# Kernel optimization log

Hardware: AMD Instinct MI355X
Metric: run time of the kernel (lower is better)

Reference implementation:

```python
import jax, jax.numpy as jnp
import numpy as np

H, DK, DV = 16, 128, 128
BINS = 64
EPS = 1e-6
NORM_EPS = 1e-5


def silu(x):
    return x * jax.nn.sigmoid(x)


def short_conv(x, w):
    # causal depthwise conv over time + silu. x: [B,T,C], w: [C,K]
    C = x.shape[-1]
    K = w.shape[1]
    lhs = jnp.swapaxes(x, 1, 2)              # [B,C,T]
    rhs = w[:, None, :]                      # [C,1,K]
    out = jax.lax.conv_general_dilated(
        lhs, rhs, window_strides=(1,), padding=[(K - 1, 0)],
        dimension_numbers=('NCH', 'OIH', 'NCH'), feature_group_count=C)
    return silu(jnp.swapaxes(out, 1, 2))


def delta_rule(q, k, v, beta, decay):
    # gated delta-rule linear attention recurrence.
    # q,k: [B,T,H,DK], v: [B,T,H,DV], beta: [B,T,H], decay: [B,T,H,DK]
    B = q.shape[0]

    def step(S, inp):
        qt, kt, vt, bt, gt = inp             # [B,H,DK],...,[B,H],[B,H,DK]
        Sd = S * gt[..., None]               # per-key-channel decay
        v_pred = jnp.einsum('bhk,bhkv->bhv', kt, Sd)
        S_new = Sd + jnp.einsum('bhk,bhv->bhkv', kt * bt[..., None], vt - v_pred)
        ot = jnp.einsum('bhk,bhkv->bhv', qt, S_new)
        return S_new, ot

    tm = lambda a: jnp.swapaxes(a, 0, 1)     # time-major
    S0 = jnp.zeros((B, H, DK, DV), q.dtype)
    _, o = jax.lax.scan(step, S0, (tm(q), tm(k), tm(v), tm(beta), tm(decay)))
    return jnp.swapaxes(o, 0, 1)             # [B,T,H,DV]


def _forward(hidden_states, wq, wk, wv, conv_q_w, conv_k_w, conv_v_w, A_log, dt_bias,
             proxy_w, unc_w, head_embed, mlp_w1, mlp_b1, mlp_w2, mlp_b2,
             bb_w, bb_b, bd_w, bd_b, lam_w, lam_b, ab_w, ab_b, ad_w, ad_b,
             g1_w, g2_w, g2_b, onorm_w, wo):
    x = hidden_states
    B, T, _ = x.shape
    q = short_conv(x @ wq, conv_q_w).reshape(B, T, H, DK)
    k = short_conv(x @ wk, conv_k_w).reshape(B, T, H, DK)
    v = short_conv(x @ wv, conv_v_w).reshape(B, T, H, DV)

    # uncertainty (entropy of predicted-token distribution proxy)
    logp = jax.nn.log_softmax(x @ unc_w, axis=-1)
    entropy = -jnp.sum(jnp.exp(logp) * logp, axis=-1)              # [B,T]
    ent_norm = entropy / jnp.log(jnp.asarray(BINS, x.dtype))

    # beta-norm: unit-norm keys inside the kernel
    k_unit = k / (jnp.linalg.norm(k, axis=-1, keepdims=True) + EPS)

    # proxy-value surprise features, per head/token
    v_hat = jnp.einsum('bthk,kv->bthv', k, proxy_w)
    err = v - v_hat
    err_n = jnp.linalg.norm(err, axis=-1)                          # [B,T,H]
    v_n = jnp.linalg.norm(v, axis=-1)
    vh_n = jnp.linalg.norm(v_hat, axis=-1)
    rel_err = err_n / (v_n + EPS)
    cos = jnp.sum(v * v_hat, axis=-1) / (v_n * vh_n + EPS)
    feats = jnp.stack([jnp.broadcast_to(ent_norm[..., None], err_n.shape),
                       rel_err, cos, jnp.log1p(err_n)], axis=-1)    # [B,T,H,4]
    he = jnp.broadcast_to(head_embed[None, None], (B, T, H, head_embed.shape[-1]))
    feats = jnp.concatenate([feats, he], axis=-1)                   # [B,T,H,8]

    hf = silu(silu(feats @ mlp_w1 + mlp_b1) @ mlp_w2 + mlp_b2)      # [B,T,H,32]
    beta_base = hf @ bb_w + bb_b[0]
    beta_delta = hf @ bd_w + bd_b[0]
    beta_fast = jax.nn.sigmoid(beta_base + beta_delta)              # fast memory: bigger step
    beta_slow = jax.nn.sigmoid(beta_base - beta_delta)              # slow memory: smaller step
    lam = jax.nn.sigmoid(hf @ lam_w + lam_b[0])                     # mixing gate
    amp_base = hf @ ab_w + ab_b[0]
    amp_delta = hf @ ad_w + ad_b[0]
    amp_fast = jax.nn.sigmoid(amp_base + amp_delta)
    amp_slow = jax.nn.sigmoid(amp_base - amp_delta)

    # KDA-style per-key-channel log-decay: g = -exp(A_log) * softplus(dt_bias)
    g_chan = -jnp.exp(A_log)[:, None] * jax.nn.softplus(dt_bias).reshape(H, DK)
    decay_fast = jnp.exp(g_chan[None, None] * amp_fast[..., None])  # [B,T,H,DK]
    decay_slow = jnp.exp(g_chan[None, None] * amp_slow[..., None])

    qs = q * (DK ** -0.5)
    o_fast = delta_rule(qs, k_unit, v, beta_fast, decay_fast)
    o_slow = delta_rule(qs, k_unit, v, beta_slow, decay_slow)
    o = lam[..., None] * o_fast + (1.0 - lam[..., None]) * o_slow   # [B,T,H,DV]

    # gated RMSNorm (sigmoid gate) + output projection
    g = ((x @ g1_w) @ g2_w + g2_b).reshape(B, T, H, DV)
    rms = jnp.sqrt(jnp.mean(o * o, axis=-1, keepdims=True) + NORM_EPS)
    o = (o / rms) * onorm_w * jax.nn.sigmoid(g)
    return o.reshape(B, T, H * DV) @ wo


def setup_inputs() -> dict:
    key = jax.random.key(0)
    ks = jax.random.split(key, 40)
    B, T, D = 2, 256, 2048

    def w(k, shape, fan_in):
        return jax.random.normal(k, shape, jnp.float32) * (fan_in ** -0.5)

    return {
        'hidden_states': jax.random.normal(ks[0], (B, T, D), jnp.float32),
        'wq': w(ks[1], (D, H * DK), D),
        'wk': w(ks[2], (D, H * DK), D),
        'wv': w(ks[3], (D, H * DV), D),
        'conv_q_w': w(ks[4], (H * DK, 4), 4),
        'conv_k_w': w(ks[5], (H * DK, 4), 4),
        'conv_v_w': w(ks[6], (H * DV, 4), 4),
        'A_log': jnp.log(jax.random.uniform(ks[7], (H,), jnp.float32, 1.0, 16.0)),
        'dt_bias': jnp.zeros((H * DK,), jnp.float32),
        'proxy_w': w(ks[8], (DK, DV), DK),
        'unc_w': w(ks[9], (D, BINS), D),
        'head_embed': jax.random.normal(ks[10], (H, 4), jnp.float32),
        'mlp_w1': w(ks[11], (8, 32), 8),
        'mlp_b1': jnp.zeros((32,), jnp.float32),
        'mlp_w2': w(ks[12], (32, 32), 32),
        'mlp_b2': jnp.zeros((32,), jnp.float32),
        'bb_w': w(ks[13], (32,), 32), 'bb_b': jnp.zeros((1,), jnp.float32),
        'bd_w': w(ks[14], (32,), 32), 'bd_b': jnp.zeros((1,), jnp.float32),
        'lam_w': w(ks[15], (32,), 32), 'lam_b': jnp.zeros((1,), jnp.float32),
        'ab_w': w(ks[16], (32,), 32), 'ab_b': jnp.zeros((1,), jnp.float32),
        'ad_w': w(ks[17], (32,), 32), 'ad_b': jnp.zeros((1,), jnp.float32),
        'g1_w': w(ks[18], (D, DV), D),
        'g2_w': w(ks[19], (DV, H * DV), DV),
        'g2_b': jnp.zeros((H * DV,), jnp.float32),
        'onorm_w': jnp.ones((DV,), jnp.float32),
        'wo': w(ks[20], (H * DV, D), H * DV),
    }


def reference(hidden_states, wq, wk, wv, conv_q_w, conv_k_w, conv_v_w, A_log, dt_bias,
              proxy_w, unc_w, head_embed, mlp_w1, mlp_b1, mlp_w2, mlp_b2,
              bb_w, bb_b, bd_w, bd_b, lam_w, lam_b, ab_w, ab_b, ad_w, ad_b,
              g1_w, g2_w, g2_b, onorm_w, wo):
    return _forward(hidden_states, wq, wk, wv, conv_q_w, conv_k_w, conv_v_w, A_log,
                    dt_bias, proxy_w, unc_w, head_embed, mlp_w1, mlp_b1, mlp_w2, mlp_b2,
                    bb_w, bb_b, bd_w, bd_b, lam_w, lam_b, ab_w, ab_b, ad_w, ad_b,
                    g1_w, g2_w, g2_b, onorm_w, wo)
```

## Files before the change

### kernel.cpp

```cpp
#include <hip/hip_runtime.h>
#include <hip/hip_bf16.h>
#include <math.h>

#define H_ 16
#define DK_ 128
#define DV_ 128
#define D_ 2048
#define T_ 256
#define B_ 2
#define BT_ 512

typedef __attribute__((ext_vector_type(8))) short short8v;
typedef __attribute__((ext_vector_type(4))) float float4v;
typedef unsigned short ushort_t;

__device__ __forceinline__ float sigmoidf_(float x){ return 1.f/(1.f+expf(-x)); }
__device__ __forceinline__ float siluf_(float x){ return x/(1.f+expf(-x)); }
__device__ __forceinline__ ushort_t f2bf(float f){
    __hip_bfloat16 h = __float2bfloat16(f);
    return *reinterpret_cast<ushort_t*>(&h);
}
__device__ __forceinline__ int swz(int row, int k){
    return row * 32 + ((((k >> 3) ^ (row & 3)) << 3) | (k & 7));
}

template<int CTRL>
__device__ __forceinline__ float ror_add_(float x){
    return x + __int_as_float(__builtin_amdgcn_update_dpp(
        0, __float_as_int(x), CTRL, 0xF, 0xF, true));
}
__device__ __forceinline__ float rsum16_(float x){
    x = ror_add_<0x121>(x);
    x = ror_add_<0x122>(x);
    x = ror_add_<0x124>(x);
    x = ror_add_<0x128>(x);
    return x;
}

__global__ void cvt_gchan(const float* __restrict__ in, ushort_t* __restrict__ out, int n,
                          const float* __restrict__ A_log, const float* __restrict__ dt_bias,
                          float* __restrict__ gchan)
{
    int bid = blockIdx.x;
    if (bid < 1024) {
        int i = (bid * 256 + threadIdx.x) * 4;
        if (i >= n) return;
        float4 v = *(const float4*)&in[i];
        union { ushort_t s[4]; unsigned long long u; } p;
        p.s[0] = f2bf(v.x); p.s[1] = f2bf(v.y); p.s[2] = f2bf(v.z); p.s[3] = f2bf(v.w);
        *(unsigned long long*)&out[i] = p.u;
    } else {
        int i = (bid - 1024) * 256 + threadIdx.x;
        int h = i >> 7;
        float x = dt_bias[i];
        float sp = (x > 20.f) ? x : log1pf(expf(x));
        gchan[i] = -expf(A_log[h]) * sp * 1.44269504088896f;
    }
}

__device__ __forceinline__ void gemm_core(
    const ushort_t* __restrict__ A, int K,
    const float* __restrict__ W, int Nst, int nloc0,
    float* __restrict__ C, int Cst, int m0, int n0out)
{
    __shared__ ushort_t Asub[2048];
    __shared__ ushort_t Bsub[2048];
    const int tid = threadIdx.x;
    const int wid = tid >> 6, lane = tid & 63;
    const int wr = (wid >> 1) * 32, wc = (wid & 1) * 32;
    const int lr = lane & 15, lk = (lane >> 4) * 8;
    const int rowA = tid >> 2, kqA = tid & 3;
    const int nW = tid & 63, kqW = tid >> 6;

    float4v acc[2][2];
    #pragma unroll
    for (int i = 0; i < 2; ++i)
        #pragma unroll
        for (int j = 0; j < 2; ++j) acc[i][j] = (float4v){0.f, 0.f, 0.f, 0.f};

    short8v aRa, aRb;
    float wRa[8], wRb[8];

#define LOADT(AR, WR, KOFF) do {                                                   \
    AR = *(const short8v*)&A[(size_t)(m0 + rowA) * K + (KOFF) + kqA * 8];          \
    _Pragma("unroll")                                                              \
    for (int r = 0; r < 8; ++r)                                                    \
        WR[r] = W[(size_t)((KOFF) + kqW * 8 + r) * Nst + nloc0 + nW];              \
} while (0)
#define STORET(AR, WR) do {                                                        \
    *(short8v*)&Asub[swz(rowA, kqA * 8)] = AR;                                     \
    union { ushort_t s[8]; short8v v; } pk;                                        \
    _Pragma("unroll")                                                              \
    for (int r = 0; r < 8; ++r) pk.s[r] = f2bf(WR[r]);                             \
    *(short8v*)&Bsub[swz(nW, kqW * 8)] = pk.v;                                     \
} while (0)
#define FRAGMMA() do {                                                             \
    short8v af0 = *(const short8v*)&Asub[swz(wr + lr, lk)];                        \
    short8v af1 = *(const short8v*)&Asub[swz(wr + 16 + lr, lk)];                   \
    short8v bf0 = *(const short8v*)&Bsub[swz(wc + lr, lk)];                        \
    short8v bf1 = *(const short8v*)&Bsub[swz(wc + 16 + lr, lk)];                   \
    acc[0][0] = __builtin_amdgcn_mfma_f32_16x16x32_bf16(af0, bf0, acc[0][0],0,0,0);\
    acc[0][1] = __builtin_amdgcn_mfma_f32_16x16x32_bf16(af0, bf1, acc[0][1],0,0,0);\
    acc[1][0] = __builtin_amdgcn_mfma_f32_16x16x32_bf16(af1, bf0, acc[1][0],0,0,0);\
    acc[1][1] = __builtin_amdgcn_mfma_f32_16x16x32_bf16(af1, bf1, acc[1][1],0,0,0);\
} while (0)

    LOADT(aRa, wRa, 0);
    for (int k0 = 0; k0 < K; k0 += 64) {
        STORET(aRa, wRa);
        __syncthreads();
        if (k0 + 32 < K) LOADT(aRb, wRb, k0 + 32);
        FRAGMMA();
        __syncthreads();
        STORET(aRb, wRb);
        __syncthreads();
        if (k0 + 64 < K) LOADT(aRa, wRa, k0 + 64);
        FRAGMMA();
        __syncthreads();
    }
#undef LOADT
#undef STORET
#undef FRAGMMA
    const int lq = (lane >> 4) * 4;
    #pragma unroll
    for (int mi = 0; mi < 2; ++mi)
        #pragma unroll
        for (int ni = 0; ni < 2; ++ni)
            #pragma unroll
            for (int j = 0; j < 4; ++j)
                C[(size_t)(m0 + wr + mi * 16 + lq + j) * Cst + (n0out + wc + ni * 16 + lr)]
                    = acc[mi][ni][j];
}

__device__ __forceinline__ void gemm_core2(
    const ushort_t* __restrict__ A, int K,
    const float* __restrict__ W, int Nst, int nloc0,
    float* __restrict__ C, int Cst, int m0, int n0out)
{
    __shared__ ushort_t Asub[8192];
    __shared__ ushort_t Bsub[2048];
    const int tid = threadIdx.x;
    const int wid = tid >> 6, lane = tid & 63;
    const int wr = wid * 32;
    const int lr = lane & 15, lk = (lane >> 4) * 8;
    const int rowA = tid >> 2;
    const int kqA  = (tid & 3) * 8;
    const int nW = tid & 63, kqW = (tid >> 6) & 3;
    const bool doW = tid < 256;

    float4v acc[2][4];
    #pragma unroll
    for (int i = 0; i < 2; ++i)
        #pragma unroll
        for (int j = 0; j < 4; ++j) acc[i][j] = (float4v){0.f, 0.f, 0.f, 0.f};

    short8v a0a, a1a, a0b, a1b;
    float wRa[8], wRb[8];

#define LOADT2(A0, A1, WR, KOFF) do {                                              \
    A0 = *(const short8v*)&A[(size_t)(m0 + rowA) * K + (KOFF) + kqA];              \
    A1 = *(const short8v*)&A[(size_t)(m0 + rowA + 128) * K + (KOFF) + kqA];        \
    if (doW) {                                                                     \
        _Pragma("unroll")                                                          \
        for (int r = 0; r < 8; ++r)                                                \
            WR[r] = W[(size_t)((KOFF) + kqW * 8 + r) * Nst + nloc0 + nW];          \
    }                                                                              \
} while (0)
#define STORET2(A0, A1, WR) do {                                                   \
    *(short8v*)&Asub[swz(rowA, kqA)] = A0;                                         \
    *(short8v*)&Asub[swz(rowA + 128, kqA)] = A1;                                   \
    if (doW) {                                                                     \
        union { ushort_t s[8]; short8v v; } pk;                                    \
        _Pragma("unroll")                                                          \
        for (int r = 0; r < 8; ++r) pk.s[r] = f2bf(WR[r]);                         \
        *(short8v*)&Bsub[swz(nW, kqW * 8)] = pk.v;                                 \
    }                                                                              \
} while (0)
#define FRAGMMA2() do {                                                            \
    short8v af0 = *(const short8v*)&Asub[swz(wr + lr, lk)];                        \
    short8v af1 = *(const short8v*)&Asub[swz(wr + 16 + lr, lk)];                   \
    short8v bf0 = *(const short8v*)&Bsub[swz(lr, lk)];                             \
    short8v bf1 = *(const short8v*)&Bsub[swz(16 + lr, lk)];                        \
    short8v bf2 = *(const short8v*)&Bsub[swz(32 + lr, lk)];                        \
    short8v bf3 = *(const short8v*)&Bsub[swz(48 + lr, lk)];                        \
    acc[0][0] = __builtin_amdgcn_mfma_f32_16x16x32_bf16(af0, bf0, acc[0][0],0,0,0);\
    acc[0][1] = __builtin_amdgcn_mfma_f32_16x16x32_bf16(af0, bf1, acc[0][1],0,0,0);\
    acc[0][2] = __builtin_amdgcn_mfma_f32_16x16x32_bf16(af0, bf2, acc[0][2],0,0,0);\
    acc[0][3] = __builtin_amdgcn_mfma_f32_16x16x32_bf16(af0, bf3, acc[0][3],0,0,0);\
    acc[1][0] = __builtin_amdgcn_mfma_f32_16x16x32_bf16(af1, bf0, acc[1][0],0,0,0);\
    acc[1][1] = __builtin_amdgcn_mfma_f32_16x16x32_bf16(af1, bf1, acc[1][1],0,0,0);\
    acc[1][2] = __builtin_amdgcn_mfma_f32_16x16x32_bf16(af1, bf2, acc[1][2],0,0,0);\
    acc[1][3] = __builtin_amdgcn_mfma_f32_16x16x32_bf16(af1, bf3, acc[1][3],0,0,0);\
} while (0)

    LOADT2(a0a, a1a, wRa, 0);
    for (int k0 = 0; k0 < K; k0 += 64) {
        STORET2(a0a, a1a, wRa);
        __syncthreads();
        if (k0 + 32 < K) LOADT2(a0b, a1b, wRb, k0 + 32);
        FRAGMMA2();
        __syncthreads();
        STORET2(a0b, a1b, wRb);
        __syncthreads();
        if (k0 + 64 < K) LOADT2(a0a, a1a, wRa, k0 + 64);
        FRAGMMA2();
        __syncthreads();
    }
#undef LOADT2
#undef STORET2
#undef FRAGMMA2
    const int lq = (lane >> 4) * 4;
    #pragma unroll
    for (int mi = 0; mi < 2; ++mi)
        #pragma unroll
        for (int ni = 0; ni < 4; ++ni)
            #pragma unroll
            for (int j = 0; j < 4; ++j)
                C[(size_t)(m0 + wr + mi * 16 + lq + j) * Cst + (n0out + ni * 16 + lr)]
                    = acc[mi][ni][j];
}

__global__ __launch_bounds__(512) void gemm_proj(const ushort_t* __restrict__ A,
    const float* __restrict__ wq, const float* __restrict__ wk, const float* __restrict__ wv,
    const float* __restrict__ unc, const float* __restrict__ g1, float* __restrict__ C)
{
    int n0 = blockIdx.x * 64, m0 = blockIdx.y * 256;
    const float* W; int nloc, Nst;
    if (n0 < 2048)      { W = wq;  nloc = n0;        Nst = 2048; }
    else if (n0 < 4096) { W = wk;  nloc = n0 - 2048; Nst = 2048; }
    else if (n0 < 6144) { W = wv;  nloc = n0 - 4096; Nst = 2048; }
    else if (n0 < 6208) { W = unc; nloc = n0 - 6144; Nst = 64; }
    else                { W = g1;  nloc = n0 - 6208; Nst = 128; }
    gemm_core2(A, 2048, W, Nst, nloc, C, 6336, m0, n0);
}

__global__ __launch_bounds__(256) void gemm_one(const ushort_t* __restrict__ A,
    const float* __restrict__ W, float* __restrict__ C, int N, int K)
{
    gemm_core(A, K, W, N, blockIdx.x * 64, C, N, blockIdx.y * 64, blockIdx.x * 64);
}

__global__ __launch_bounds__(256) void gemm_g2(const float* __restrict__ Cb,
    const float* __restrict__ W, float* __restrict__ C)
{
    __shared__ ushort_t Asub[2048];
    __shared__ ushort_t Bsub[2048];
    const int tid = threadIdx.x;
    const int wid = tid >> 6, lane = tid & 63;
    const int wr = (wid >> 1) * 32, wc = (wid & 1) * 32;
    const int lr = lane & 15, lk = (lane >> 4) * 8;
    const int rowA = tid >> 2, kqA = (tid & 3) * 8;
    const int nW = tid & 63, kqW = tid >> 6;
    const int m0 = blockIdx.y * 64, n0 = blockIdx.x * 64;

    float4v acc[2][2];
    #pragma unroll
    for (int i = 0; i < 2; ++i)
        #pragma unroll
        for (int j = 0; j < 2; ++j) acc[i][j] = (float4v){0.f, 0.f, 0.f, 0.f};

    for (int k0 = 0; k0 < 128; k0 += 32) {
        const float* asrc = &Cb[(size_t)(m0 + rowA) * 6336 + 6208 + k0 + kqA];
        float4 a4a = *(const float4*)asrc;
        float4 a4b = *(const float4*)(asrc + 4);
        float w8[8];
        #pragma unroll
        for (int r = 0; r < 8; ++r)
            w8[r] = W[(size_t)(k0 + kqW * 8 + r) * 2048 + n0 + nW];
        __syncthreads();
        union { ushort_t s[8]; short8v v; } pa, pw;
        pa.s[0]=f2bf(a4a.x); pa.s[1]=f2bf(a4a.y); pa.s[2]=f2bf(a4a.z); pa.s[3]=f2bf(a4a.w);
        pa.s[4]=f2bf(a4b.x); pa.s[5]=f2bf(a4b.y); pa.s[6]=f2bf(a4b.z); pa.s[7]=f2bf(a4b.w);
        *(short8v*)&Asub[swz(rowA, kqA)] = pa.v;
        #pragma unroll
        for (int r = 0; r < 8; ++r) pw.s[r] = f2bf(w8[r]);
        *(short8v*)&Bsub[swz(nW, kqW * 8)] = pw.v;
        __syncthreads();
        short8v af0 = *(const short8v*)&Asub[swz(wr + lr, lk)];
        short8v af1 = *(const short8v*)&Asub[swz(wr + 16 + lr, lk)];
        short8v bf0 = *(const short8v*)&Bsub[swz(wc + lr, lk)];
        short8v bf1 = *(const short8v*)&Bsub[swz(wc + 16 + lr, lk)];
        acc[0][0] = __builtin_amdgcn_mfma_f32_16x16x32_bf16(af0, bf0, acc[0][0],0,0,0);
        acc[0][1] = __builtin_amdgcn_mfma_f32_16x16x32_bf16(af0, bf1, acc[0][1],0,0,0);
        acc[1][0] = __builtin_amdgcn_mfma_f32_16x16x32_bf16(af1, bf0, acc[1][0],0,0,0);
        acc[1][1] = __builtin_amdgcn_mfma_f32_16x16x32_bf16(af1, bf1, acc[1][1],0,0,0);
    }
    const int lq = (lane >> 4) * 4;
    #pragma unroll
    for (int mi = 0; mi < 2; ++mi)
        #pragma unroll
        for (int ni = 0; ni < 2; ++ni)
            #pragma unroll
            for (int j = 0; j < 4; ++j)
                C[(size_t)(m0 + wr + mi * 16 + lq + j) * 2048 + (n0 + wc + ni * 16 + lr)]
                    = acc[mi][ni][j];
}

__global__ void conv_fused(const float* __restrict__ Cb,
    const float* __restrict__ wq, const float* __restrict__ wk, const float* __restrict__ wv,
    float* __restrict__ qc, float* __restrict__ kc, float* __restrict__ vc,
    ushort_t* __restrict__ kcb, float qscale)
{
    int c  = blockIdx.x * 256 + threadIdx.x;
    int bt = blockIdx.y;
    int b  = bt / T_, t = bt % T_;
    int which = c >> 11, cloc = c & 2047;
    const float* w = which == 0 ? wq : which == 1 ? wk : wv;
    float* o = which == 0 ? qc : which == 1 ? kc : vc;
    float scale = which == 0 ? qscale : 1.f;
    float acc = 0.f;
    #pragma unroll
    for (int j = 0; j < 4; ++j) {
        int tt = t - 3 + j;
        if (tt >= 0) acc = fmaf(w[cloc * 4 + j], Cb[((size_t)(b * T_ + tt)) * 6336 + c], acc);
    }
    float r = siluf_(acc) * scale;
    o[(size_t)bt * D_ + cloc] = r;
    if (which == 1) kcb[(size_t)bt * D_ + cloc] = f2bf(r);
}

__global__ __launch_bounds__(128) void featsprec_k(
    const float* __restrict__ kc, const float* __restrict__ vc,
    const float* __restrict__ qc,
    const float* __restrict__ vhatA, const float* __restrict__ Cb,
    const float* __restrict__ he, const float* __restrict__ gchan,
    const float* __restrict__ w1, const float* __restrict__ b1,
    const float* __restrict__ w2, const float* __restrict__ b2,
    const float* __restrict__ bbw, const float* __restrict__ bbb,
    const float* __restrict__ bdw, const float* __restrict__ bdb,
    const float* __restrict__ lamw, const float* __restrict__ lamb,
    const float* __restrict__ abw, const float* __restrict__ abb,
    const float* __restrict__ adw, const float* __restrict__ adb,
    float* __restrict__ lm, float* __restrict__ kuA,
    float* __restrict__ dA, float4* __restrict__ scal4A)
{
    int blk = blockIdx.x;
    int h = blk & 15, bt = blk >> 4;
    int b = bt / T_, t = bt % T_;
    int v = threadIdx.x;
    __shared__ float part[2][5];
    __shared__ float tot5[5];
    __shared__ float feats8[8];
    __shared__ float hf1[32];
    __shared__ float hf[32];
    __shared__ float entSh;
    __shared__ float scal5[5];

    if (v < 64) {
        float x = Cb[(size_t)bt * 6336 + 6144 + v];
        float m = x;
        #pragma unroll
        for (int o = 32; o > 0; o >>= 1) m = fmaxf(m, __shfl_xor(m, o));
        float e = expf(x - m);
        float s = e;
        #pragma unroll
        for (int o = 32; o > 0; o >>= 1) s += __shfl_xor(s, o);
        float lp = (x - m) - logf(s);
        float c = -expf(lp) * lp;
        #pragma unroll
        for (int o = 32; o > 0; o >>= 1) c += __shfl_xor(c, o);
        if (v == 0) entSh = c / logf(64.f);
    }

    size_t base = (size_t)bt * D_ + h * 128;
    float kval = kc[base + v];
    float vval = vc[base + v];
    float vhat = vhatA[(size_t)blk * 128 + v];

    float e = vval - vhat;
    float sums[5] = {kval * kval, vval * vval, vhat * vhat, vval * vhat, e * e};
    #pragma unroll
    for (int i = 0; i < 5; ++i) {
        float s = sums[i];
        #pragma unroll
        for (int o = 32; o > 0; o >>= 1) s += __shfl_xor(s, o);
        if ((threadIdx.x & 63) == 0) part[threadIdx.x >> 6][i] = s;
    }
    __syncthreads();
    if (threadIdx.x < 5) tot5[threadIdx.x] = part[0][threadIdx.x] + part[1][threadIdx.x];
    __syncthreads();
    if (threadIdx.x == 0) {
        float k2 = tot5[0], v2 = tot5[1], vh2 = tot5[2], vvh = tot5[3], e2 = tot5[4];
        float knorm = sqrtf(k2);
        float err_n = sqrtf(e2);
        float v_n = sqrtf(v2);
        float vh_n = sqrtf(vh2);
        feats8[0] = entSh;
        feats8[1] = err_n / (v_n + 1e-6f);
        feats8[2] = vvh / (v_n * vh_n + 1e-6f);
        feats8[3] = log1pf(err_n);
        feats8[4] = he[h * 4 + 0];
        feats8[5] = he[h * 4 + 1];
        feats8[6] = he[h * 4 + 2];
        feats8[7] = he[h * 4 + 3];
        scal5[4] = knorm;
    }
    __syncthreads();
    if (threadIdx.x < 32) {
        float a = b1[threadIdx.x];
        #pragma unroll
        for (int j = 0; j < 8; ++j) a = fmaf(feats8[j], w1[j * 32 + threadIdx.x], a);
        hf1[threadIdx.x] = siluf_(a);
    }
    __syncthreads();
    if (threadIdx.x < 32) {
        float a = b2[threadIdx.x];
        #pragma unroll
        for (int j = 0; j < 32; ++j) a = fmaf(hf1[j], w2[j * 32 + threadIdx.x], a);
        hf[threadIdx.x] = siluf_(a);
    }
    __syncthreads();
    if (threadIdx.x == 0) {
        float bb = bbb[0], bd = bdb[0], lv = lamb[0], ab = abb[0], ad = adb[0];
        #pragma unroll
        for (int j = 0; j < 32; ++j) {
            float hj = hf[j];
            bb = fmaf(hj, bbw[j], bb);
            bd = fmaf(hj, bdw[j], bd);
            lv = fmaf(hj, lamw[j], lv);
            ab = fmaf(hj, abw[j], ab);
            ad = fmaf(hj, adw[j], ad);
        }
        scal5[0] = sigmoidf_(bb + bd);
        scal5[1] = sigmoidf_(bb - bd);
        scal5[2] = sigmoidf_(ab + ad);
        scal5[3] = sigmoidf_(ab - ad);
        lm[((size_t)(b * H_ + h)) * T_ + t] = sigmoidf_(lv);
    }
    __syncthreads();

    const float bfv = scal5[0], bsv = scal5[1];
    const float afv = scal5[2], asv = scal5[3], knv = scal5[4];
    const int k = threadIdx.x;
    const int bh = b * 16 + h;
    float gch = gchan[h * 128 + k];
    float kuv = kval / (knv + 1e-6f);
    kuA[((size_t)bh * 256 + t) * 128 + k] = kuv;
    dA[((size_t)bh * 256 + t) * 128 + k]        = exp2f(gch * afv);
    dA[((size_t)(32 + bh) * 256 + t) * 128 + k] = exp2f(gch * asv);
    float pq = qc[base + k] * kuv;
    #pragma unroll
    for (int o = 32; o > 0; o >>= 1) pq += __shfl_xor(pq, o);
    if ((threadIdx.x & 63) == 0) part[threadIdx.x >> 6][0] = pq;
    __syncthreads();
    if (threadIdx.x == 0) {
        float pt = part[0][0] + part[1][0];
        float4 s0; s0.x = afv; s0.y = bfv; s0.z = pt * bfv; s0.w = 0.f;
        float4 s1; s1.x = asv; s1.y = bsv; s1.z = pt * bsv; s1.w = 0.f;
        scal4A[(size_t)bh * 256 + t] = s0;
        scal4A[(size_t)(32 + bh) * 256 + t] = s1;
    }
}

struct OPS { float4 a0, a1, q0, q1, d0, d1, sc; float2 vv; };

__global__ __launch_bounds__(256) void delta_wave9(
    const float* __restrict__ qc, const float* __restrict__ vc,
    const float* __restrict__ kuA, const float* __restrict__ dA,
    const float4* __restrict__ scal4A,
    float* __restrict__ o_fast, float* __restrict__ o_slow)
{
    const int p  = blockIdx.x;
    const int lb = (p & 7) * 32 + (p >> 3);
    const int bh = lb >> 3, rule = (lb >> 2) & 1, vq = lb & 3;
    const int b = bh >> 4, h = bh & 15;
    const int rbh = rule * 32 + bh;
    const int tid = threadIdx.x;
    const int wid = tid >> 6, lane = tid & 63;
    const int kl = lane & 15, vg = lane >> 4;
    const int vloc = wid * 8 + vg * 2;
    const int vcol = vq * 32 + vloc;

    __shared__ float kuL[2][16][144];
    __shared__ float qL [2][16][144];
    __shared__ float dL [2][16][144];
    __shared__ float vL [2][16][32];
    __shared__ float scL[2][16][4];

    const float*  __restrict__ pkuG = kuA + (size_t)bh * 256 * 128;
    const float*  __restrict__ pdG  = dA + (size_t)rbh * 256 * 128;
    const float*  __restrict__ pqG  = qc + (size_t)b * T_ * D_ + h * 128;
    const float*  __restrict__ pvG  = vc + (size_t)b * T_ * D_ + h * 128 + vq * 32;
    const float4* __restrict__ pscG = scal4A + (size_t)rbh * 256;
    float* __restrict__ obase = (rule ? o_slow : o_fast)
                                + (size_t)b * T_ * D_ + h * 128 + vcol;

    const int srow = (tid & 127) >> 3;
    const int scol = (tid & 7) * 16;
    const bool isK = tid < 128;
    const int ck0 = scol >> 3;
    const int fo_w0 = ck0 * 8 + (ck0 >> 2) * 4;
    const int fo_w1 = (ck0 + 1) * 8 + ((ck0 + 1) >> 2) * 4;

    float4 sb0, sb1, sb2, sb3, svb, ssc, sd0, sd1;

    float S[8][2];
    #pragma unroll
    for (int j = 0; j < 8; ++j) { S[j][0] = 0.f; S[j][1] = 0.f; }

#define STAGE_LOAD(C) do {                                                         \
    const int t0_ = (C) * 16;                                                      \
    const float* dsrc = pdG + (size_t)(t0_ + srow) * 128 + scol;                   \
    if (isK) {                                                                     \
        const float* src = pkuG + (size_t)(t0_ + srow) * 128 + scol;               \
        sb0 = *(const float4*)(src);      sb1 = *(const float4*)(src + 4);         \
        sb2 = *(const float4*)(src + 8);  sb3 = *(const float4*)(src + 12);        \
        svb = *(const float4*)(pvG + (size_t)(t0_ + srow) * D_ + (tid & 7) * 4);   \
        sd0 = *(const float4*)(dsrc);     sd1 = *(const float4*)(dsrc + 4);        \
    } else {                                                                       \
        const float* src = pqG + (size_t)(t0_ + srow) * D_ + scol;                 \
        sb0 = *(const float4*)(src);      sb1 = *(const float4*)(src + 4);         \
        sb2 = *(const float4*)(src + 8);  sb3 = *(const float4*)(src + 12);        \
        sd0 = *(const float4*)(dsrc + 8); sd1 = *(const float4*)(dsrc + 12);       \
        if ((tid & 127) < 16) ssc = *(const float4*)&pscG[t0_ + (tid & 127)];      \
    }                                                                              \
} while (0)

#define STAGE_WRITE(BI) do {                                                       \
    if (isK) {                                                                     \
        *(float4*)&kuL[BI][srow][fo_w0]     = sb0;                                 \
        *(float4*)&kuL[BI][srow][fo_w0 + 4] = sb1;                                 \
        *(float4*)&kuL[BI][srow][fo_w1]     = sb2;                                 \
        *(float4*)&kuL[BI][srow][fo_w1 + 4] = sb3;                                 \
        *(float4*)&vL[BI][srow][(tid & 7) * 4] = svb;                              \
        *(float4*)&dL[BI][srow][fo_w0]      = sd0;                                 \
        *(float4*)&dL[BI][srow][fo_w0 + 4]  = sd1;                                 \
    } else {                                                                       \
        *(float4*)&qL[BI][srow][fo_w0]     = sb0;                                  \
        *(float4*)&qL[BI][srow][fo_w0 + 4] = sb1;                                  \
        *(float4*)&qL[BI][srow][fo_w1]     = sb2;                                  \
        *(float4*)&qL[BI][srow][fo_w1 + 4] = sb3;                                  \
        *(float4*)&dL[BI][srow][fo_w1]      = sd0;                                 \
        *(float4*)&dL[BI][srow][fo_w1 + 4]  = sd1;                                 \
        if ((tid & 127) < 16) *(float4*)&scL[BI][tid & 127][0] = ssc;              \
    }                                                                              \
} while (0)

#define LDOPS(R, BI, TS) do {                                                      \
    R.a0 = *(const float4*)&kuL[BI][TS][fo];                                       \
    R.a1 = *(const float4*)&kuL[BI][TS][fo + 4];                                   \
    R.q0 = *(const float4*)&qL[BI][TS][fo];                                        \
    R.q1 = *(const float4*)&qL[BI][TS][fo + 4];                                    \
    R.d0 = *(const float4*)&dL[BI][TS][fo];                                        \
    R.d1 = *(const float4*)&dL[BI][TS][fo + 4];                                    \
    R.vv = *(const float2*)&vL[BI][TS][vloc];                                      \
    R.sc = *(const float4*)&scL[BI][TS][0];                                        \
} while (0)

#define STEP(TT, CUR, NXT, BI) do {                                                \
    if ((TT) + 1 < 16) LDOPS(NXT, BI, (TT) + 1);                                   \
    float ku[8] = {CUR.a0.x, CUR.a0.y, CUR.a0.z, CUR.a0.w,                         \
                   CUR.a1.x, CUR.a1.y, CUR.a1.z, CUR.a1.w};                        \
    float qv[8] = {CUR.q0.x, CUR.q0.y, CUR.q0.z, CUR.q0.w,                         \
                   CUR.q1.x, CUR.q1.y, CUR.q1.z, CUR.q1.w};                        \
    float d[8]  = {CUR.d0.x, CUR.d0.y, CUR.d0.z, CUR.d0.w,                         \
                   CUR.d1.x, CUR.d1.y, CUR.d1.z, CUR.d1.w};                        \
    float vp0a = 0.f, vp0b = 0.f, vp1a = 0.f, vp1b = 0.f;                          \
    float oq0a = 0.f, oq0b = 0.f, oq1a = 0.f, oq1b = 0.f;                          \
    _Pragma("unroll")                                                              \
    for (int j = 0; j < 4; ++j) {                                                  \
        float kudA = ku[j] * d[j],     qdA = qv[j] * d[j];                         \
        float kudB = ku[j+4] * d[j+4], qdB = qv[j+4] * d[j+4];                     \
        vp0a = fmaf(kudA, S[j][0], vp0a);   vp0b = fmaf(kudB, S[j+4][0], vp0b);    \
        vp1a = fmaf(kudA, S[j][1], vp1a);   vp1b = fmaf(kudB, S[j+4][1], vp1b);    \
        oq0a = fmaf(qdA,  S[j][0], oq0a);   oq0b = fmaf(qdB,  S[j+4][0], oq0b);    \
        oq1a = fmaf(qdA,  S[j][1], oq1a);   oq1b = fmaf(qdB,  S[j+4][1], oq1b);    \
    }                                                                              \
    float vp0 = rsum16_(vp0a + vp0b);                                              \
    float vp1 = rsum16_(vp1a + vp1b);                                              \
    float oq0 = rsum16_(oq0a + oq0b);                                              \
    float oq1 = rsum16_(oq1a + oq1b);                                              \
    float dv0 = CUR.vv.x - vp0, dv1 = CUR.vv.y - vp1;                              \
    float o0 = fmaf(CUR.sc.z, dv0, oq0);                                           \
    float o1 = fmaf(CUR.sc.z, dv1, oq1);                                           \
    float bd0 = CUR.sc.y * dv0, bd1 = CUR.sc.y * dv1;                              \
    _Pragma("unroll")                                                              \
    for (int j = 0; j < 8; ++j) {                                                  \
        S[j][0] = fmaf(d[j], S[j][0], ku[j] * bd0);                                \
        S[j][1] = fmaf(d[j], S[j][1], ku[j] * bd1);                                \
    }                                                                              \
    if (kl == 0) {                                                                 \
        float2 ov; ov.x = o0; ov.y = o1;                                           \
        *(float2*)&obase[(size_t)(tb + (TT)) * D_] = ov;                           \
    }                                                                              \
} while (0)

    const int fo = kl * 8 + (kl >> 2) * 4;

    STAGE_LOAD(0);
    STAGE_WRITE(0);
    __syncthreads();

    OPS rA, rB;
    for (int c = 0; c < 16; ++c) {
        if (c < 15) STAGE_LOAD(c + 1);
        const int bi = c & 1;
        const int tb = c * 16;
        LDOPS(rA, bi, 0);
        #pragma unroll
        for (int ts = 0; ts < 16; ts += 2) {
            STEP(ts,     rA, rB, bi);
            STEP(ts + 1, rB, rA, bi);
        }
        if (c < 15) STAGE_WRITE((c + 1) & 1);
        __syncthreads();
    }
#undef STAGE_LOAD
#undef STAGE_WRITE
#undef LDOPS
#undef STEP
}

__global__ __launch_bounds__(128) void combine_k(
    const float* __restrict__ of, const float* __restrict__ os,
    const float* __restrict__ lm, const float* __restrict__ graw,
    const float* __restrict__ g2b, const float* __restrict__ onw,
    ushort_t* __restrict__ ocb)
{
    int blk = blockIdx.x;
    int h = blk & 15, bt = blk >> 4;
    int b = bt / T_, t = bt % T_;
    int v = threadIdx.x;
    size_t idx = (size_t)bt * D_ + h * 128 + v;
    float l = lm[((size_t)(b * H_ + h)) * T_ + t];
    float o = l * of[idx] + (1.f - l) * os[idx];
    float s = o * o;
    #pragma unroll
    for (int off = 32; off > 0; off >>= 1) s += __shfl_xor(s, off);
    __shared__ float ws2[2];
    if ((threadIdx.x & 63) == 0) ws2[threadIdx.x >> 6] = s;
    __syncthreads();
    float tot = ws2[0] + ws2[1];
    float rms = sqrtf(tot / 128.f + 1e-5f);
    float g = graw[idx] + g2b[h * 128 + v];
    ocb[idx] = f2bf(o / rms * onw[v] * sigmoidf_(g));
}

extern "C" void kernel_launch(void* const* d_in, const int* in_sizes, int n_in,
                              void* d_out, int out_size, void* d_ws, size_t ws_size,
                              hipStream_t stream)
{
    const float* x        = (const float*)d_in[0];
    const float* wq       = (const float*)d_in[1];
    const float* wk       = (const float*)d_in[2];
    const float* wv       = (const float*)d_in[3];
    const float* conv_q_w = (const float*)d_in[4];
    const float* conv_k_w = (const float*)d_in[5];
    const float* conv_v_w = (const float*)d_in[6];
    const float* A_log    = (const float*)d_in[7];
    const float* dt_bias  = (const float*)d_in[8];
    const float* proxy_w  = (const float*)d_in[9];
    const float* unc_w    = (const float*)d_in[10];
    const float* he       = (const float*)d_in[11];
    const float* mlp_w1   = (const float*)d_in[12];
    const float* mlp_b1   = (const float*)d_in[13];
    const float* mlp_w2   = (const float*)d_in[14];
    const float* mlp_b2   = (const float*)d_in[15];
    const float* bb_w     = (const float*)d_in[16];
    const float* bb_b     = (const float*)d_in[17];
    const float* bd_w     = (const float*)d_in[18];
    const float* bd_b     = (const float*)d_in[19];
    const float* lam_w    = (const float*)d_in[20];
    const float* lam_b    = (const float*)d_in[21];
    const float* ab_w     = (const float*)d_in[22];
    const float* ab_b     = (const float*)d_in[23];
    const float* ad_w     = (const float*)d_in[24];
    const float* ad_b     = (const float*)d_in[25];
    const float* g1_w     = (const float*)d_in[26];
    const float* g2_w     = (const float*)d_in[27];
    const float* g2_b     = (const float*)d_in[28];
    const float* onorm_w  = (const float*)d_in[29];
    const float* wo       = (const float*)d_in[30];
    float* out = (float*)d_out;

    float* ws = (float*)d_ws;
    const size_t SZ = (size_t)BT_ * D_;
    float* C_big = ws;
    float* qc    = C_big + (size_t)512 * 6336;
    float* kc    = qc + SZ;
    float* vc    = kc + SZ;
    float* graw  = vc + SZ;
    float* lm    = graw + SZ;
    float* gchan = lm + 8192;
    float* scal4 = gchan + 2048;
    float* kuA   = scal4 + 65536;
    float* dA    = kuA + 1048576;
    float* vhatA = dA + 2097152;
    float* fend  = vhatA + 1048576;
    ushort_t* xb = (ushort_t*)fend;

    float* o_fast  = C_big;
    float* o_slow  = C_big + SZ;
    ushort_t* ocb  = xb;
    ushort_t* kcb  = (ushort_t*)dA;

    dim3 blk256(256);
    dim3 blk512(512);
    const float QSCALE = 0.08838834764831845f;

    cvt_gchan<<<dim3(1032), blk256, 0, stream>>>(x, xb, (int)SZ, A_log, dt_bias, gchan);
    gemm_proj<<<dim3(99, 2), blk512, 0, stream>>>(xb, wq, wk, wv, unc_w, g1_w, C_big);
    gemm_g2<<<dim3(32, 8), blk256, 0, stream>>>(C_big, g2_w, graw);
    conv_fused<<<dim3(24, BT_), blk256, 0, stream>>>(C_big, conv_q_w, conv_k_w, conv_v_w,
                                                     qc, kc, vc, kcb, QSCALE);
    gemm_one<<<dim3(2, 128), blk256, 0, stream>>>(kcb, proxy_w, vhatA, 128, 128);
    featsprec_k<<<dim3(BT_ * H_), dim3(128), 0, stream>>>(
        kc, vc, qc, vhatA, C_big, he, gchan,
        mlp_w1, mlp_b1, mlp_w2, mlp_b2,
        bb_w, bb_b, bd_w, bd_b, lam_w, lam_b, ab_w, ab_b, ad_w, ad_b,
        lm, kuA, dA, (float4*)scal4);
    delta_wave9<<<dim3(256), blk256, 0, stream>>>(qc, vc, kuA, dA,
                                                  (const float4*)scal4,
                                                  o_fast, o_slow);
    combine_k<<<dim3(BT_ * H_), dim3(128), 0, stream>>>(o_fast, o_slow, lm, graw,
                                                        g2_b, onorm_w, ocb);
    gemm_one<<<dim3(32, 8), blk256, 0, stream>>>(ocb, wo, out, 2048, 2048);
}
```

Before: 210.6 us.

## Fuse g2 gating GEMM into delta-rule kernel as extra blocks

Removes the separate gemm_g2 launch and runs its 256 tiles as additional blocks (index >= 256) of the delta-rule kernel, so the GEMM fills idle CUs while the 256 recurrence blocks run. The outputs o_fast and o_slow are moved to the kc and vhatA buffers, because C_big is still being read by the GEMM blocks. The per-step scalar record in shared memory shrinks from float4 to float2. The cost is a larger shared-memory union that every block reserves, and a tail that now depends on how blocks are scheduled.

After: 206.5 us, median of 2. Within noise of the previous version (-1.9%).

```diff
diff --git a/kernel.cpp b/kernel.cpp
--- a/kernel.cpp
+++ b/kernel.cpp
@@ -240,62 +240,6 @@
     gemm_core(A, K, W, N, blockIdx.x * 64, C, N, blockIdx.y * 64, blockIdx.x * 64);
 }
 
-__global__ __launch_bounds__(256) void gemm_g2(const float* __restrict__ Cb,
-    const float* __restrict__ W, float* __restrict__ C)
-{
-    __shared__ ushort_t Asub[2048];
-    __shared__ ushort_t Bsub[2048];
-    const int tid = threadIdx.x;
-    const int wid = tid >> 6, lane = tid & 63;
-    const int wr = (wid >> 1) * 32, wc = (wid & 1) * 32;
-    const int lr = lane & 15, lk = (lane >> 4) * 8;
-    const int rowA = tid >> 2, kqA = (tid & 3) * 8;
-    const int nW = tid & 63, kqW = tid >> 6;
-    const int m0 = blockIdx.y * 64, n0 = blockIdx.x * 64;
-
-    float4v acc[2][2];
-    #pragma unroll
-    for (int i = 0; i < 2; ++i)
-        #pragma unroll
-        for (int j = 0; j < 2; ++j) acc[i][j] = (float4v){0.f, 0.f, 0.f, 0.f};
-
-    for (int k0 = 0; k0 < 128; k0 += 32) {
-        const float* asrc = &Cb[(size_t)(m0 + rowA) * 6336 + 6208 + k0 + kqA];
-        float4 a4a = *(const float4*)asrc;
-        float4 a4b = *(const float4*)(asrc + 4);
-        float w8[8];
-        #pragma unroll
-        for (int r = 0; r < 8; ++r)
-            w8[r] = W[(size_t)(k0 + kqW * 8 + r) * 2048 + n0 + nW];
-        __syncthreads();
-        union { ushort_t s[8]; short8v v; } pa, pw;
-        pa.s[0]=f2bf(a4a.x); pa.s[1]=f2bf(a4a.y); pa.s[2]=f2bf(a4a.z); pa.s[3]=f2bf(a4a.w);
-        pa.s[4]=f2bf(a4b.x); pa.s[5]=f2bf(a4b.y); pa.s[6]=f2bf(a4b.z); pa.s[7]=f2bf(a4b.w);
-        *(short8v*)&Asub[swz(rowA, kqA)] = pa.v;
-        #pragma unroll
-        for (int r = 0; r < 8; ++r) pw.s[r] = f2bf(w8[r]);
-        *(short8v*)&Bsub[swz(nW, kqW * 8)] = pw.v;
-        __syncthreads();
-        short8v af0 = *(const short8v*)&Asub[swz(wr + lr, lk)];
-        short8v af1 = *(const short8v*)&Asub[swz(wr + 16 + lr, lk)];
-        short8v bf0 = *(const short8v*)&Bsub[swz(wc + lr, lk)];
-        short8v bf1 = *(const short8v*)&Bsub[swz(wc + 16 + lr, lk)];
-        acc[0][0] = __builtin_amdgcn_mfma_f32_16x16x32_bf16(af0, bf0, acc[0][0],0,0,0);
-        acc[0][1] = __builtin_amdgcn_mfma_f32_16x16x32_bf16(af0, bf1, acc[0][1],0,0,0);
-        acc[1][0] = __builtin_amdgcn_mfma_f32_16x16x32_bf16(af1, bf0, acc[1][0],0,0,0);
-        acc[1][1] = __builtin_amdgcn_mfma_f32_16x16x32_bf16(af1, bf1, acc[1][1],0,0,0);
-    }
-    const int lq = (lane >> 4) * 4;
-    #pragma unroll
-    for (int mi = 0; mi < 2; ++mi)
-        #pragma unroll
-        for (int ni = 0; ni < 2; ++ni)
-            #pragma unroll
-            for (int j = 0; j < 4; ++j)
-                C[(size_t)(m0 + wr + mi * 16 + lq + j) * 2048 + (n0 + wc + ni * 16 + lr)]
-                    = acc[mi][ni][j];
-}
-
 __global__ void conv_fused(const float* __restrict__ Cb,
     const float* __restrict__ wq, const float* __restrict__ wk, const float* __restrict__ wv,
     float* __restrict__ qc, float* __restrict__ kc, float* __restrict__ vc,
@@ -452,30 +396,89 @@
     }
 }
 
-struct OPS { float4 a0, a1, q0, q1, d0, d1, sc; float2 vv; };
-
-__global__ __launch_bounds__(256) void delta_wave9(
+struct OPS { float4 a0, a1, q0, q1, d0, d1; float2 vv, sc2; };
+
+__global__ __launch_bounds__(256) void delta_g2_fused(
     const float* __restrict__ qc, const float* __restrict__ vc,
     const float* __restrict__ kuA, const float* __restrict__ dA,
     const float4* __restrict__ scal4A,
-    float* __restrict__ o_fast, float* __restrict__ o_slow)
-{
+    float* __restrict__ o_fast, float* __restrict__ o_slow,
+    const float* __restrict__ Cb, const float* __restrict__ g2w,
+    float* __restrict__ graw)
+{
+    __shared__ __align__(16) char smem[59648];
+    const int tid = threadIdx.x;
+
+    if (blockIdx.x >= 256) {
+        ushort_t* Asub = (ushort_t*)smem;
+        ushort_t* Bsub = (ushort_t*)(smem + 4096);
+        const int p2 = blockIdx.x - 256;
+        const int m0 = (p2 >> 5) * 64, n0 = (p2 & 31) * 64;
+        const int wid = tid >> 6, lane = tid & 63;
+        const int wr = (wid >> 1) * 32, wc = (wid & 1) * 32;
+        const int lr = lane & 15, lk = (lane >> 4) * 8;
+        const int rowA = tid >> 2, kqA = (tid & 3) * 8;
+        const int nW = tid & 63, kqW = tid >> 6;
+
+        float4v acc[2][2];
+        #pragma unroll
+        for (int i = 0; i < 2; ++i)
+            #pragma unroll
+            for (int j = 0; j < 2; ++j) acc[i][j] = (float4v){0.f, 0.f, 0.f, 0.f};
+
+        for (int k0 = 0; k0 < 128; k0 += 32) {
+            const float* asrc = &Cb[(size_t)(m0 + rowA) * 6336 + 6208 + k0 + kqA];
+            float4 a4a = *(const float4*)asrc;
+            float4 a4b = *(const float4*)(asrc + 4);
+            float w8[8];
+            #pragma unroll
+            for (int r = 0; r < 8; ++r)
+                w8[r] = g2w[(size_t)(k0 + kqW * 8 + r) * 2048 + n0 + nW];
+            __syncthreads();
+            union { ushort_t s[8]; short8v v; } pa, pw;
+            pa.s[0]=f2bf(a4a.x); pa.s[1]=f2bf(a4a.y); pa.s[2]=f2bf(a4a.z); pa.s[3]=f2bf(a4a.w);
+            pa.s[4]=f2bf(a4b.x); pa.s[5]=f2bf(a4b.y); pa.s[6]=f2bf(a4b.z); pa.s[7]=f2bf(a4b.w);
+            *(short8v*)&Asub[swz(rowA, kqA)] = pa.v;
+            #pragma unroll
+            for (int r = 0; r < 8; ++r) pw.s[r] = f2bf(w8[r]);
+            *(short8v*)&Bsub[swz(nW, kqW * 8)] = pw.v;
+            __syncthreads();
+            short8v af0 = *(const short8v*)&Asub[swz(wr + lr, lk)];
+            short8v af1 = *(const short8v*)&Asub[swz(wr + 16 + lr, lk)];
+            short8v bf0 = *(const short8v*)&Bsub[swz(wc + lr, lk)];
+            short8v bf1 = *(const short8v*)&Bsub[swz(wc + 16 + lr, lk)];
+            acc[0][0] = __builtin_amdgcn_mfma_f32_16x16x32_bf16(af0, bf0, acc[0][0],0,0,0);
+            acc[0][1] = __builtin_amdgcn_mfma_f32_16x16x32_bf16(af0, bf1, acc[0][1],0,0,0);
+            acc[1][0] = __builtin_amdgcn_mfma_f32_16x16x32_bf16(af1, bf0, acc[1][0],0,0,0);
+            acc[1][1] = __builtin_amdgcn_mfma_f32_16x16x32_bf16(af1, bf1, acc[1][1],0,0,0);
+        }
+        const int lq = (lane >> 4) * 4;
+        #pragma unroll
+        for (int mi = 0; mi < 2; ++mi)
+            #pragma unroll
+            for (int ni = 0; ni < 2; ++ni)
+                #pragma unroll
+                for (int j = 0; j < 4; ++j)
+                    graw[(size_t)(m0 + wr + mi * 16 + lq + j) * 2048 + (n0 + wc + ni * 16 + lr)]
+                        = acc[mi][ni][j];
+        return;
+    }
+
+    float (*kuL)[16][144] = (float (*)[16][144])(smem);
+    float (*qL)[16][144]  = (float (*)[16][144])(smem + 18432);
+    float (*dL)[16][144]  = (float (*)[16][144])(smem + 36864);
+    float (*vL)[16][32]   = (float (*)[16][32])(smem + 55296);
+    float (*scL)[16][2]   = (float (*)[16][2])(smem + 59392);
+
     const int p  = blockIdx.x;
     const int lb = (p & 7) * 32 + (p >> 3);
     const int bh = lb >> 3, rule = (lb >> 2) & 1, vq = lb & 3;
     const int b = bh >> 4, h = bh & 15;
     const int rbh = rule * 32 + bh;
-    const int tid = threadIdx.x;
     const int wid = tid >> 6, lane = tid & 63;
     const int kl = lane & 15, vg = lane >> 4;
     const int vloc = wid * 8 + vg * 2;
     const int vcol = vq * 32 + vloc;
-
-    __shared__ float kuL[2][16][144];
-    __shared__ float qL [2][16][144];
-    __shared__ float dL [2][16][144];
-    __shared__ float vL [2][16][32];
-    __shared__ float scL[2][16][4];
 
     const float*  __restrict__ pkuG = kuA + (size_t)bh * 256 * 128;
     const float*  __restrict__ pdG  = dA + (size_t)rbh * 256 * 128;
@@ -532,7 +535,10 @@
         *(float4*)&qL[BI][srow][fo_w1 + 4] = sb3;                                  \
         *(float4*)&dL[BI][srow][fo_w1]      = sd0;                                 \
         *(float4*)&dL[BI][srow][fo_w1 + 4]  = sd1;                                 \
-        if ((tid & 127) < 16) *(float4*)&scL[BI][tid & 127][0] = ssc;              \
+        if ((tid & 127) < 16) {                                                    \
+            float2 w2_; w2_.x = ssc.y; w2_.y = ssc.z;                              \
+            *(float2*)&scL[BI][tid & 127][0] = w2_;                                \
+        }                                                                          \
     }                                                                              \
 } while (0)
 
@@ -544,7 +550,7 @@
     R.d0 = *(const float4*)&dL[BI][TS][fo];                                        \
     R.d1 = *(const float4*)&dL[BI][TS][fo + 4];                                    \
     R.vv = *(const float2*)&vL[BI][TS][vloc];                                      \
-    R.sc = *(const float4*)&scL[BI][TS][0];                                        \
+    R.sc2 = *(const float2*)&scL[BI][TS][0];                                       \
 } while (0)
 
 #define STEP(TT, CUR, NXT, BI) do {                                                \
@@ -571,9 +577,9 @@
     float oq0 = rsum16_(oq0a + oq0b);                                              \
     float oq1 = rsum16_(oq1a + oq1b);                                              \
     float dv0 = CUR.vv.x - vp0, dv1 = CUR.vv.y - vp1;                              \
-    float o0 = fmaf(CUR.sc.z, dv0, oq0);                                           \
-    float o1 = fmaf(CUR.sc.z, dv1, oq1);                                           \
-    float bd0 = CUR.sc.y * dv0, bd1 = CUR.sc.y * dv1;                              \
+    float o0 = fmaf(CUR.sc2.y, dv0, oq0);                                          \
+    float o1 = fmaf(CUR.sc2.y, dv1, oq1);                                          \
+    float bd0 = CUR.sc2.x * dv0, bd1 = CUR.sc2.x * dv1;                            \
     _Pragma("unroll")                                                              \
     for (int j = 0; j < 8; ++j) {                                                  \
         S[j][0] = fmaf(d[j], S[j][0], ku[j] * bd0);                                \
@@ -689,8 +695,8 @@
     float* fend  = vhatA + 1048576;
     ushort_t* xb = (ushort_t*)fend;
 
-    float* o_fast  = C_big;
-    float* o_slow  = C_big + SZ;
+    float* o_fast  = kc;
+    float* o_slow  = vhatA;
     ushort_t* ocb  = xb;
     ushort_t* kcb  = (ushort_t*)dA;
 
@@ -700,7 +706,6 @@
 
     cvt_gchan<<<dim3(1032), blk256, 0, stream>>>(x, xb, (int)SZ, A_log, dt_bias, gchan);
     gemm_proj<<<dim3(99, 2), blk512, 0, stream>>>(xb, wq, wk, wv, unc_w, g1_w, C_big);
-    gemm_g2<<<dim3(32, 8), blk256, 0, stream>>>(C_big, g2_w, graw);
     conv_fused<<<dim3(24, BT_), blk256, 0, stream>>>(C_big, conv_q_w, conv_k_w, conv_v_w,
                                                      qc, kc, vc, kcb, QSCALE);
     gemm_one<<<dim3(2, 128), blk256, 0, stream>>>(kcb, proxy_w, vhatA, 128, 128);
@@ -709,9 +714,10 @@
         mlp_w1, mlp_b1, mlp_w2, mlp_b2,
         bb_w, bb_b, bd_w, bd_b, lam_w, lam_b, ab_w, ab_b, ad_w, ad_b,
         lm, kuA, dA, (float4*)scal4);
-    delta_wave9<<<dim3(256), blk256, 0, stream>>>(qc, vc, kuA, dA,
-                                                  (const float4*)scal4,
-                                                  o_fast, o_slow);
+    delta_g2_fused<<<dim3(512), blk256, 0, stream>>>(qc, vc, kuA, dA,
+                                                     (const float4*)scal4,
+                                                     o_fast, o_slow,
+                                                     C_big, g2_w, graw);
     combine_k<<<dim3(BT_ * H_), dim3(128), 0, stream>>>(o_fast, o_slow, lm, graw,
                                                         g2_b, onorm_w, ocb);
     gemm_one<<<dim3(32, 8), blk256, 0, stream>>>(ocb, wo, out, 2048, 2048);
```
